# Optimization experiments

Measured on AMD Instinct MI355X. Metric: run time of the kernel, lower is better.

## Reference

```python
import jax, jax.numpy as jnp
import numpy as np

N_P, N_A = 100000, 20000
F_P, D_A, H = 512, 128, 256
E_W, E_C = 200000, 400000


def setup_inputs() -> dict:
    key = jax.random.key(0)
    ks = jax.random.split(key, 32)
    s = 0.05  # param init scale
    inp = {
        # node inputs
        'paper_feat': (jax.random.uniform(ks[0], (N_P, F_P)) < 0.02).astype(jnp.float32),  # sparse multi-hot
        'author_emb': jax.random.normal(ks[1], (N_A, D_A), jnp.float32),
        # edges: author --writes--> paper, paper --cites--> paper
        'writes_src': jax.random.randint(ks[2], (E_W,), 0, N_A, jnp.int32),
        'writes_dst': jax.random.randint(ks[3], (E_W,), 0, N_P, jnp.int32),
        'writes_w': jax.random.uniform(ks[4], (E_W,), jnp.float32),
        'cites_src': jax.random.randint(ks[5], (E_C,), 0, N_P, jnp.int32),
        'cites_dst': jax.random.randint(ks[6], (E_C,), 0, N_P, jnp.int32),
        'cites_w': jax.random.uniform(ks[7], (E_C,), jnp.float32),
        # layer 1 params (in dims per node type: paper=F_P, author=D_A)
        'W1_self_p': jax.random.normal(ks[8], (F_P, H), jnp.float32) * s,
        'b1_self_p': jnp.zeros((H,), jnp.float32),
        'W1_self_a': jax.random.normal(ks[9], (D_A, H), jnp.float32) * s,
        'b1_self_a': jnp.zeros((H,), jnp.float32),
        'W1_rel_writes': jax.random.normal(ks[10], (D_A, H), jnp.float32) * s,
        'b1_rel_writes': jnp.zeros((H,), jnp.float32),
        'W1_rel_cites': jax.random.normal(ks[11], (F_P, H), jnp.float32) * s,
        'b1_rel_cites': jnp.zeros((H,), jnp.float32),
        # layer 2 params (all in dims = H)
        'W2_self_p': jax.random.normal(ks[12], (H, H), jnp.float32) * s,
        'b2_self_p': jnp.zeros((H,), jnp.float32),
        'W2_self_a': jax.random.normal(ks[13], (H, H), jnp.float32) * s,
        'b2_self_a': jnp.zeros((H,), jnp.float32),
        'W2_rel_writes': jax.random.normal(ks[14], (H, H), jnp.float32) * s,
        'b2_rel_writes': jnp.zeros((H,), jnp.float32),
        'W2_rel_cites': jax.random.normal(ks[15], (H, H), jnp.float32) * s,
        'b2_rel_cites': jnp.zeros((H,), jnp.float32),
    }
    return inp


def _hetero_layer(xp, xa, edges, Wsp, bsp, Wsa, bsa, Wrw, brw, Wrc, brc, activation):
    """One HeteroLayer: per-type self linear + per-relation gather/scale/scatter-add."""
    writes_src, writes_dst, writes_w, cites_src, cites_dst, cites_w = edges
    out_p = xp @ Wsp + bsp          # [N_P, H]
    out_a = xa @ Wsa + bsa          # [N_A, H]
    # relation author --writes--> paper
    msg_w = xa @ Wrw + brw          # dense per-relation linear on source nodes
    gathered_w = msg_w[writes_src] * writes_w[:, None]          # gather + edge weight
    out_p = out_p + jax.ops.segment_sum(gathered_w, writes_dst, num_segments=out_p.shape[0])
    # relation paper --cites--> paper
    msg_c = xp @ Wrc + brc
    gathered_c = msg_c[cites_src] * cites_w[:, None]
    out_p = out_p + jax.ops.segment_sum(gathered_c, cites_dst, num_segments=out_p.shape[0])
    if activation:
        out_p = jax.nn.elu(out_p)
        out_a = jax.nn.elu(out_a)
    return out_p, out_a


def reference(paper_feat, author_emb,
              writes_src, writes_dst, writes_w,
              cites_src, cites_dst, cites_w,
              W1_self_p, b1_self_p, W1_self_a, b1_self_a,
              W1_rel_writes, b1_rel_writes, W1_rel_cites, b1_rel_cites,
              W2_self_p, b2_self_p, W2_self_a, b2_self_a,
              W2_rel_writes, b2_rel_writes, W2_rel_cites, b2_rel_cites):
    edges = (writes_src, writes_dst, writes_w, cites_src, cites_dst, cites_w)
    xp, xa = _hetero_layer(paper_feat, author_emb, edges,
                           W1_self_p, b1_self_p, W1_self_a, b1_self_a,
                           W1_rel_writes, b1_rel_writes, W1_rel_cites, b1_rel_cites,
                           activation=True)
    xp, xa = _hetero_layer(xp, xa, edges,
                           W2_self_p, b2_self_p, W2_self_a, b2_self_a,
                           W2_rel_writes, b2_rel_writes, W2_rel_cites, b2_rel_cites,
                           activation=False)
    return xp, xa
```

## Files before the change

kernel.cpp:

```cpp
#include <hip/hip_runtime.h>
#include <cstdint>
#include <cstddef>

constexpr int Hd  = 256;
constexpr int N_P = 100000;
constexpr int N_A = 20000;
constexpr int F_P = 512;
constexpr int D_A = 128;

typedef short bf16x8 __attribute__((ext_vector_type(8)));
typedef float f32x4  __attribute__((ext_vector_type(4)));

__device__ inline unsigned short f2b(float x) {
    unsigned u = __float_as_uint(x);
    u += 0x7fffu + ((u >> 16) & 1u);
    return (unsigned short)(u >> 16);
}
__device__ inline float b2f(unsigned short h) {
    return __uint_as_float((unsigned)h << 16);
}

__device__ inline void bsplit(float x, unsigned short& hi, unsigned short& lo) {
    const unsigned u = __float_as_uint(x);
    hi = (unsigned short)(u >> 16);
    const float r = x - __uint_as_float(u & 0xffff0000u);
    lo = (unsigned short)(__float_as_uint(r) >> 16);
}

__global__ void prep_kernel(const float* __restrict__ W1sa, const float* __restrict__ W1rw,
                            const float* __restrict__ W2sa, const float* __restrict__ W2rw,
                            const float* __restrict__ W2rc, const float* __restrict__ W2sp,
                            const float* __restrict__ b1sa, const float* __restrict__ b1rw,
                            const float* __restrict__ b2sa, const float* __restrict__ b2rw,
                            const float* __restrict__ b2rc, const float* __restrict__ b2sp,
                            unsigned short* __restrict__ w1h,  unsigned short* __restrict__ w1l,
                            unsigned short* __restrict__ wA2h, unsigned short* __restrict__ wA2l,
                            unsigned short* __restrict__ wP2h, unsigned short* __restrict__ wP2l,
                            float* __restrict__ bc1, float* __restrict__ bcA2,
                            float* __restrict__ bcP2) {
    const int b = blockIdx.x;
    if (b < 640) {
        const float *Wa, *Wb; unsigned short *wh, *wl; int rel;
        if (b < 128)      { Wa = W1sa; Wb = W1rw; wh = w1h;  wl = w1l;  rel = b; }
        else if (b < 384) { Wa = W2sa; Wb = W2rw; wh = wA2h; wl = wA2l; rel = b - 128; }
        else              { Wa = W2rc; Wb = W2sp; wh = wP2h; wl = wP2l; rel = b - 384; }
        const int ks  = rel >> 5;
        const int nfg = rel & 31;
        const int l   = threadIdx.x;
        const float* W = (nfg < 16) ? Wa : Wb;
        const int col  = (nfg & 15) * 16 + (l & 15);
        const size_t base = ((size_t)rel * 64 + l) * 8;
        #pragma unroll
        for (int j = 0; j < 8; ++j) {
            const int k = ks * 32 + ((l >> 4) * 8) + j;
            unsigned short h, lw;
            bsplit(W[(size_t)k * Hd + col], h, lw);
            wh[base + j] = h;
            wl[base + j] = lw;
        }
    } else {
        const int t     = (b - 640) * 64 + threadIdx.x;
        const int which = t >> 9;
        const int idx   = t & 511;
        const float* src; float* dst;
        if (which == 0)      { src = (idx < 256) ? b1sa : b1rw; dst = bc1; }
        else if (which == 1) { src = (idx < 256) ? b2sa : b2rw; dst = bcA2; }
        else                 { src = (idx < 256) ? b2rc : b2sp; dst = bcP2; }
        dst[idx] = src[idx & 255];
    }
}

__global__ void mfma_dual_kernel(const float* __restrict__ A, const int K,
                                 const unsigned short* __restrict__ whi,
                                 const unsigned short* __restrict__ wlo,
                                 const float* __restrict__ bcat,
                                 void* __restrict__ Oa, void* __restrict__ Ob,
                                 const int actA, const int actB,
                                 const int bfA, const int bfB) {
    extern __shared__ char smem[];
    char* sh = smem;
    char* sl = smem + 32 * K * 2;
    const int  tid = threadIdx.x;
    const int  wid = tid >> 6;
    const int  l   = tid & 63;
    const long m0  = (long)blockIdx.x * 32;
    const int  rowStride = 2 * K;

    const int kq4 = K >> 2;
    for (int i = tid; i < 32 * kq4; i += 256) {
        const int row = i / kq4;
        const int kq  = i - row * kq4;
        const float4 v = *(const float4*)(A + (m0 + row) * K + kq * 4);
        unsigned short h0, h1, h2, h3, l0, l1, l2, l3;
        bsplit(v.x, h0, l0); bsplit(v.y, h1, l1);
        bsplit(v.z, h2, l2); bsplit(v.w, h3, l3);
        int ofs = row * rowStride + ((kq * 8) ^ ((row & 7) << 4));
        *(ushort4*)(sh + ofs) = make_ushort4(h0, h1, h2, h3);
        *(ushort4*)(sl + ofs) = make_ushort4(l0, l1, l2, l3);
    }
    __syncthreads();

    f32x4 acc[2][8];
    #pragma unroll
    for (int nf = 0; nf < 8; ++nf) {
        const float b = bcat[wid * 128 + nf * 16 + (l & 15)];
        acc[0][nf] = (f32x4){b, b, b, b};
        acc[1][nf] = (f32x4){b, b, b, b};
    }

    const int kb  = (l >> 4) * 16;
    const int r0  = l & 15;
    const int r1  = 16 + r0;
    const int sw  = (l & 7) << 4;
    const int ro0 = r0 * rowStride;
    const int ro1 = r1 * rowStride;
    for (int ks = 0; ks < (K >> 5); ++ks) {
        const int bk = (ks * 64 + kb) ^ sw;
        const bf16x8 ah0 = *(const bf16x8*)(sh + ro0 + bk);
        const bf16x8 al0 = *(const bf16x8*)(sl + ro0 + bk);
        const bf16x8 ah1 = *(const bf16x8*)(sh + ro1 + bk);
        const bf16x8 al1 = *(const bf16x8*)(sl + ro1 + bk);
        const size_t wbase = (((size_t)ks * 32 + wid * 8) * 64 + l) * 8;
        #pragma unroll
        for (int nf = 0; nf < 8; ++nf) {
            const bf16x8 bh = *(const bf16x8*)(whi + wbase + (size_t)nf * 512);
            const bf16x8 bl = *(const bf16x8*)(wlo + wbase + (size_t)nf * 512);
            acc[0][nf] = __builtin_amdgcn_mfma_f32_16x16x32_bf16(ah0, bh, acc[0][nf], 0, 0, 0);
            acc[1][nf] = __builtin_amdgcn_mfma_f32_16x16x32_bf16(ah1, bh, acc[1][nf], 0, 0, 0);
            acc[0][nf] = __builtin_amdgcn_mfma_f32_16x16x32_bf16(al0, bh, acc[0][nf], 0, 0, 0);
            acc[1][nf] = __builtin_amdgcn_mfma_f32_16x16x32_bf16(al1, bh, acc[1][nf], 0, 0, 0);
            acc[0][nf] = __builtin_amdgcn_mfma_f32_16x16x32_bf16(ah0, bl, acc[0][nf], 0, 0, 0);
            acc[1][nf] = __builtin_amdgcn_mfma_f32_16x16x32_bf16(ah1, bl, acc[1][nf], 0, 0, 0);
        }
    }

    #pragma unroll
    for (int mf = 0; mf < 2; ++mf) {
        #pragma unroll
        for (int nf = 0; nf < 8; ++nf) {
            const int colg = wid * 128 + nf * 16 + (l & 15);
            void* O;
            int col, act, isbf;
            if (colg < 256) { O = Oa; col = colg;       act = actA; isbf = bfA; }
            else            { O = Ob; col = colg - 256; act = actB; isbf = bfB; }
            const long row = m0 + mf * 16 + ((l >> 4) * 4);
            const f32x4 v = acc[mf][nf];
            #pragma unroll
            for (int r = 0; r < 4; ++r) {
                float x = v[r];
                if (act) x = x > 0.f ? x : expm1f(x);
                if (isbf) ((unsigned short*)O)[(row + r) * Hd + col] = f2b(x);
                else      ((float*)O)[(row + r) * Hd + col] = x;
            }
        }
    }
}

__device__ inline void walk_row(const unsigned long long* __restrict__ m,
                                const float* __restrict__ Ws,
                                const float* __restrict__ Wc,
                                const int lane, float4& accS, float4& accC) {
    float4 pS = make_float4(0.f, 0.f, 0.f, 0.f);
    float4 pC = make_float4(0.f, 0.f, 0.f, 0.f);
    #pragma unroll
    for (int g = 0; g < 8; ++g) {
        const int cbase = (g >> 2) * 256 + (g & 3);
        unsigned long long mm = m[g];
        while (mm) {
            const int bit = __ffsll((long long)mm) - 1;
            mm &= mm - 1;
            const int k = cbase + bit * 4;
            const float4 nS = ((const float4*)(Ws + (size_t)k * Hd))[lane];
            const float4 nC = ((const float4*)(Wc + (size_t)k * Hd))[lane];
            accS.x += pS.x; accS.y += pS.y; accS.z += pS.z; accS.w += pS.w;
            accC.x += pC.x; accC.y += pC.y; accC.z += pC.z; accC.w += pC.w;
            pS = nS; pC = nC;
        }
    }
    accS.x += pS.x; accS.y += pS.y; accS.z += pS.z; accS.w += pS.w;
    accC.x += pC.x; accC.y += pC.y; accC.z += pC.z; accC.w += pC.w;
}

__global__ void sparse_dual_kernel(const float* __restrict__ pf,
                                   const float* __restrict__ Ws, const float* __restrict__ bs,
                                   const float* __restrict__ Wc, const float* __restrict__ bc,
                                   float* __restrict__ outS, unsigned short* __restrict__ outC) {
    const int lane = threadIdx.x & 63;
    const int row0 = blockIdx.x * 8 + (threadIdx.x >> 6) * 2;
    const float4* p0 = (const float4*)(pf + (size_t)row0 * F_P);
    const float4* p1 = (const float4*)(pf + (size_t)(row0 + 1) * F_P);
    const float4 a0 = p0[lane], b0 = p0[64 + lane];
    const float4 a1 = p1[lane], b1 = p1[64 + lane];
    unsigned long long m0[8], m1[8];
    m0[0] = __ballot(a0.x != 0.f); m0[1] = __ballot(a0.y != 0.f);
    m0[2] = __ballot(a0.z != 0.f); m0[3] = __ballot(a0.w != 0.f);
    m0[4] = __ballot(b0.x != 0.f); m0[5] = __ballot(b0.y != 0.f);
    m0[6] = __ballot(b0.z != 0.f); m0[7] = __ballot(b0.w != 0.f);
    m1[0] = __ballot(a1.x != 0.f); m1[1] = __ballot(a1.y != 0.f);
    m1[2] = __ballot(a1.z != 0.f); m1[3] = __ballot(a1.w != 0.f);
    m1[4] = __ballot(b1.x != 0.f); m1[5] = __ballot(b1.y != 0.f);
    m1[6] = __ballot(b1.z != 0.f); m1[7] = __ballot(b1.w != 0.f);

    const float4 biasS = ((const float4*)bs)[lane];
    const float4 biasC = ((const float4*)bc)[lane];

    float4 accS = biasS, accC = biasC;
    walk_row(m0, Ws, Wc, lane, accS, accC);
    ((float4*)(outS + (size_t)row0 * Hd))[lane] = accS;
    ((ushort4*)(outC + (size_t)row0 * Hd))[lane] =
        make_ushort4(f2b(accC.x), f2b(accC.y), f2b(accC.z), f2b(accC.w));

    accS = biasS; accC = biasC;
    walk_row(m1, Ws, Wc, lane, accS, accC);
    ((float4*)(outS + (size_t)(row0 + 1) * Hd))[lane] = accS;
    ((ushort4*)(outC + (size_t)(row0 + 1) * Hd))[lane] =
        make_ushort4(f2b(accC.x), f2b(accC.y), f2b(accC.z), f2b(accC.w));
}

__global__ void hist2_kernel(const int* __restrict__ wdst, const int EW,
                             const int* __restrict__ cdst, const int EC,
                             int* __restrict__ cntW, int* __restrict__ cntC) {
    for (int i = blockIdx.x * blockDim.x + threadIdx.x; i < EW + EC; i += gridDim.x * blockDim.x) {
        if (i < EW) atomicAdd(&cntW[wdst[i]], 1);
        else        atomicAdd(&cntC[cdst[i - EW]], 1);
    }
}

__global__ void scan1_kernel(int* __restrict__ offW, int* __restrict__ offC,
                             const int n, const int nb, int* __restrict__ bsum) {
    __shared__ int s[256];
    const int sec   = (blockIdx.x < nb) ? 0 : 1;
    int* data       = sec ? offC : offW;
    const int chunk = blockIdx.x - sec * nb;
    const int t = threadIdx.x;
    const int base = chunk * 1024 + t * 4;
    int v0 = (base + 0 < n) ? data[base + 0] : 0;
    int v1 = (base + 1 < n) ? data[base + 1] : 0;
    int v2 = (base + 2 < n) ? data[base + 2] : 0;
    int v3 = (base + 3 < n) ? data[base + 3] : 0;
    const int tsum = v0 + v1 + v2 + v3;
    s[t] = tsum;
    __syncthreads();
    for (int off = 1; off < 256; off <<= 1) {
        int y = (t >= off) ? s[t - off] : 0;
        __syncthreads();
        if (t >= off) s[t] += y;
        __syncthreads();
    }
    const int e = s[t] - tsum;
    if (base + 0 < n) data[base + 0] = e;
    if (base + 1 < n) data[base + 1] = e + v0;
    if (base + 2 < n) data[base + 2] = e + v0 + v1;
    if (base + 3 < n) data[base + 3] = e + v0 + v1 + v2;
    if (t == 255) bsum[blockIdx.x] = s[255];
}

__global__ void scan2_kernel(int* __restrict__ bsum, const int nb) {
    __shared__ int s[256];
    const int t = threadIdx.x;
    int* seg = bsum + blockIdx.x * nb;
    const int v = (t < nb) ? seg[t] : 0;
    s[t] = v;
    __syncthreads();
    for (int off = 1; off < 256; off <<= 1) {
        int y = (t >= off) ? s[t - off] : 0;
        __syncthreads();
        if (t >= off) s[t] += y;
        __syncthreads();
    }
    if (t < nb) seg[t] = s[t] - v;
}

__global__ void scan3_kernel(int* __restrict__ offW, int* __restrict__ offC,
                             const int n, const int nb, const int nblk,
                             const int* __restrict__ bsum) {
    const int sec = (blockIdx.x < nblk) ? 0 : 1;
    int* data     = sec ? offC : offW;
    const int i   = (blockIdx.x - sec * nblk) * 256 + threadIdx.x;
    if (i < n) data[i] += bsum[sec * nb + (i >> 10)];
}

__global__ void fill2_kernel(const int* __restrict__ wsrc, const int* __restrict__ wdst,
                             const float* __restrict__ ww, const int EW,
                             const int* __restrict__ csrc, const int* __restrict__ cdst,
                             const float* __restrict__ cw, const int EC,
                             int* __restrict__ curW, int* __restrict__ curC,
                             int2* __restrict__ edgeW, int2* __restrict__ edgeC) {
    for (int i = blockIdx.x * blockDim.x + threadIdx.x; i < EW + EC; i += gridDim.x * blockDim.x) {
        if (i < EW) {
            const int p = atomicAdd(&curW[wdst[i]], 1);
            edgeW[p] = make_int2(wsrc[i], __float_as_int(ww[i]));
        } else {
            const int j = i - EW;
            const int p = atomicAdd(&curC[cdst[j]], 1);
            edgeC[p] = make_int2(csrc[j], __float_as_int(cw[j]));
        }
    }
}

__device__ inline void fma4(float4& acc, const float w, const ushort4 q) {
    acc.x += w * b2f(q.x); acc.y += w * b2f(q.y);
    acc.z += w * b2f(q.z); acc.w += w * b2f(q.w);
}

__device__ inline void gather_rel(float4& acc, const int lane,
                                  const unsigned short* __restrict__ m,
                                  const int2* __restrict__ earr,
                                  const int s, const int e) {
    int i = s;
    int2 e0, e1;
    if (i + 2 <= e) { e0 = earr[i]; e1 = earr[i + 1]; }
    ushort4 q0 = make_ushort4(0, 0, 0, 0), q1 = q0;
    float w0 = 0.f, w1 = 0.f;
    int havePend = 0;
    while (i + 2 <= e) {
        const ushort4 g0 = ((const ushort4*)(m + (size_t)e0.x * Hd))[lane];
        const ushort4 g1 = ((const ushort4*)(m + (size_t)e1.x * Hd))[lane];
        const float cw0 = __int_as_float(e0.y);
        const float cw1 = __int_as_float(e1.y);
        i += 2;
        if (i + 2 <= e) { e0 = earr[i]; e1 = earr[i + 1]; }
        if (havePend) { fma4(acc, w0, q0); fma4(acc, w1, q1); }
        q0 = g0; q1 = g1; w0 = cw0; w1 = cw1; havePend = 1;
    }
    if (havePend) { fma4(acc, w0, q0); fma4(acc, w1, q1); }
    for (; i < e; ++i) {
        const int2 ee = earr[i];
        const ushort4 g = ((const ushort4*)(m + (size_t)ee.x * Hd))[lane];
        fma4(acc, __int_as_float(ee.y), g);
    }
}

__global__ void aggregate_kernel(float* __restrict__ io,
                                 const unsigned short* __restrict__ mW, const int* __restrict__ offW,
                                 const int2* __restrict__ eW,
                                 const unsigned short* __restrict__ mC, const int* __restrict__ offC,
                                 const int2* __restrict__ eC,
                                 const int do_elu) {
    const int wid  = threadIdx.x >> 6;
    const int lane = threadIdx.x & 63;
    const int p    = blockIdx.x * 4 + wid;
    if (p >= N_P) return;
    float4 acc = ((const float4*)(io + (size_t)p * Hd))[lane];
    gather_rel(acc, lane, mW, eW, (p == 0) ? 0 : offW[p - 1], offW[p]);
    gather_rel(acc, lane, mC, eC, (p == 0) ? 0 : offC[p - 1], offC[p]);
    if (do_elu) {
        acc.x = acc.x > 0.f ? acc.x : expm1f(acc.x);
        acc.y = acc.y > 0.f ? acc.y : expm1f(acc.y);
        acc.z = acc.z > 0.f ? acc.z : expm1f(acc.z);
        acc.w = acc.w > 0.f ? acc.w : expm1f(acc.w);
    }
    ((float4*)(io + (size_t)p * Hd))[lane] = acc;
}

extern "C" void kernel_launch(void* const* d_in, const int* in_sizes, int n_in,
                              void* d_out, int out_size, void* d_ws, size_t ws_size,
                              hipStream_t stream) {
    const float* pf    = (const float*)d_in[0];
    const float* ae    = (const float*)d_in[1];
    const int*   wsrc  = (const int*)d_in[2];
    const int*   wdst  = (const int*)d_in[3];
    const float* ww    = (const float*)d_in[4];
    const int*   csrc  = (const int*)d_in[5];
    const int*   cdst  = (const int*)d_in[6];
    const float* cw    = (const float*)d_in[7];
    const float* W1sp  = (const float*)d_in[8];
    const float* b1sp  = (const float*)d_in[9];
    const float* W1sa  = (const float*)d_in[10];
    const float* b1sa  = (const float*)d_in[11];
    const float* W1rw  = (const float*)d_in[12];
    const float* b1rw  = (const float*)d_in[13];
    const float* W1rc  = (const float*)d_in[14];
    const float* b1rc  = (const float*)d_in[15];
    const float* W2sp  = (const float*)d_in[16];
    const float* b2sp  = (const float*)d_in[17];
    const float* W2sa  = (const float*)d_in[18];
    const float* b2sa  = (const float*)d_in[19];
    const float* W2rw  = (const float*)d_in[20];
    const float* b2rw  = (const float*)d_in[21];
    const float* W2rc  = (const float*)d_in[22];
    const float* b2rc  = (const float*)d_in[23];

    const int E_W = in_sizes[2];
    const int E_C = in_sizes[5];

    float* outP = (float*)d_out;
    float* outA = outP + (size_t)N_P * Hd;

    float*          xa1    = (float*)d_ws;
    unsigned short* msgw_b = (unsigned short*)(xa1 + (size_t)N_A * Hd);
    unsigned short* msg_b  = msgw_b + (size_t)N_A * Hd;
    int*            offW   = (int*)(msg_b + (size_t)N_P * Hd);
    int*            offC   = offW + N_P;
    int2*           edgeW  = (int2*)(offC + N_P);
    int2*           edgeC  = edgeW + E_W;
    int*            bsum   = (int*)(edgeC + E_C);
    float*          bc1    = (float*)(bsum + 512);
    float*          bcA2   = bc1 + 512;
    float*          bcP2   = bcA2 + 512;
    unsigned short* w1h    = (unsigned short*)(bcP2 + 512);
    unsigned short* w1l    = w1h  + (size_t)128 * 512;
    unsigned short* wA2h   = w1l  + (size_t)128 * 512;
    unsigned short* wA2l   = wA2h + (size_t)256 * 512;
    unsigned short* wP2h   = wA2l + (size_t)256 * 512;
    unsigned short* wP2l   = wP2h + (size_t)256 * 512;

    const dim3 blk(256);
    const int  nb   = (N_P + 1023) / 1024;
    const int  nblk = (N_P + 255) / 256;

    prep_kernel<<<664, 64, 0, stream>>>(W1sa, W1rw, W2sa, W2rw, W2rc, W2sp,
                                        b1sa, b1rw, b2sa, b2rw, b2rc, b2sp,
                                        w1h, w1l, wA2h, wA2l, wP2h, wP2l,
                                        bc1, bcA2, bcP2);

    hipMemsetAsync(offW, 0, (size_t)2 * N_P * sizeof(int), stream);
    hist2_kernel<<<1024, blk, 0, stream>>>(wdst, E_W, cdst, E_C, offW, offC);
    scan1_kernel<<<2 * nb, blk, 0, stream>>>(offW, offC, N_P, nb, bsum);
    scan2_kernel<<<2, blk, 0, stream>>>(bsum, nb);
    scan3_kernel<<<2 * nblk, blk, 0, stream>>>(offW, offC, N_P, nb, nblk, bsum);
    fill2_kernel<<<1024, blk, 0, stream>>>(wsrc, wdst, ww, E_W, csrc, cdst, cw, E_C,
                                           offW, offC, edgeW, edgeC);

    sparse_dual_kernel<<<N_P / 8, blk, 0, stream>>>(pf, W1sp, b1sp, W1rc, b1rc, outP, msg_b);
    mfma_dual_kernel<<<N_A / 32, blk, 128 * 128, stream>>>(ae, 128, w1h, w1l, bc1,
                                                           xa1, msgw_b, 1, 0, 0, 1);
    aggregate_kernel<<<(N_P + 3) / 4, blk, 0, stream>>>(outP, msgw_b, offW, edgeW,
                                                        msg_b, offC, edgeC, 1);

    mfma_dual_kernel<<<N_A / 32, blk, 128 * 256, stream>>>(xa1, 256, wA2h, wA2l, bcA2,
                                                           outA, msgw_b, 0, 0, 0, 1);
    mfma_dual_kernel<<<N_P / 32, blk, 128 * 256, stream>>>(outP, 256, wP2h, wP2l, bcP2,
                                                           msg_b, outP, 0, 0, 1, 0);
    aggregate_kernel<<<(N_P + 3) / 4, blk, 0, stream>>>(outP, msgw_b, offW, edgeW,
                                                        msg_b, offC, edgeC, 0);
}
```

Baseline: 544.5 us.

## Merge edge CSR, compact sparse nonzeros, stage edges in LDS, bf16 cites weight

The two relations' CSR structures are merged into one edge list over a concatenated author+paper message buffer. This halves the histogram, scan and fill work and gives aggregation one contiguous edge range per node. The aggregate kernel stages each block's edges in shared memory and gathers four messages per chunk with double buffering to raise memory-level parallelism. The sparse first layer packs each wave's nonzero indices for four rows into an LDS queue and walks them in pipelined chunks. It also reads a bf16 copy of W1_rel_cites, adding bf16 rounding of that weight and extra prep work.

```diff
diff --git a/kernel.cpp b/kernel.cpp
--- a/kernel.cpp
+++ b/kernel.cpp
@@ -11,16 +11,16 @@
 typedef short bf16x8 __attribute__((ext_vector_type(8)));
 typedef float f32x4  __attribute__((ext_vector_type(4)));
 
-__device__ inline unsigned short f2b(float x) {
+__device__ __forceinline__ unsigned short f2b(float x) {
     unsigned u = __float_as_uint(x);
     u += 0x7fffu + ((u >> 16) & 1u);
     return (unsigned short)(u >> 16);
 }
-__device__ inline float b2f(unsigned short h) {
+__device__ __forceinline__ float b2f(unsigned short h) {
     return __uint_as_float((unsigned)h << 16);
 }
 
-__device__ inline void bsplit(float x, unsigned short& hi, unsigned short& lo) {
+__device__ __forceinline__ void bsplit(float x, unsigned short& hi, unsigned short& lo) {
     const unsigned u = __float_as_uint(x);
     hi = (unsigned short)(u >> 16);
     const float r = x - __uint_as_float(u & 0xffff0000u);
@@ -30,12 +30,14 @@
 __global__ void prep_kernel(const float* __restrict__ W1sa, const float* __restrict__ W1rw,
                             const float* __restrict__ W2sa, const float* __restrict__ W2rw,
                             const float* __restrict__ W2rc, const float* __restrict__ W2sp,
+                            const float* __restrict__ W1rc,
                             const float* __restrict__ b1sa, const float* __restrict__ b1rw,
                             const float* __restrict__ b2sa, const float* __restrict__ b2rw,
                             const float* __restrict__ b2rc, const float* __restrict__ b2sp,
                             unsigned short* __restrict__ w1h,  unsigned short* __restrict__ w1l,
                             unsigned short* __restrict__ wA2h, unsigned short* __restrict__ wA2l,
                             unsigned short* __restrict__ wP2h, unsigned short* __restrict__ wP2l,
+                            unsigned short* __restrict__ wcb,
                             float* __restrict__ bc1, float* __restrict__ bcA2,
                             float* __restrict__ bcP2) {
     const int b = blockIdx.x;
@@ -58,8 +60,12 @@
             wh[base + j] = h;
             wl[base + j] = lw;
         }
+    } else if (b < 896) {
+        const int i0 = (b - 640) * 512 + threadIdx.x * 8;
+        #pragma unroll
+        for (int j = 0; j < 8; ++j) wcb[i0 + j] = f2b(W1rc[i0 + j]);
     } else {
-        const int t     = (b - 640) * 64 + threadIdx.x;
+        const int t     = (b - 896) * 64 + threadIdx.x;
         const int which = t >> 9;
         const int idx   = t & 511;
         const float* src; float* dst;
@@ -156,84 +162,139 @@
     }
 }
 
-__device__ inline void walk_row(const unsigned long long* __restrict__ m,
-                                const float* __restrict__ Ws,
-                                const float* __restrict__ Wc,
-                                const int lane, float4& accS, float4& accC) {
-    float4 pS = make_float4(0.f, 0.f, 0.f, 0.f);
-    float4 pC = make_float4(0.f, 0.f, 0.f, 0.f);
-    #pragma unroll
-    for (int g = 0; g < 8; ++g) {
-        const int cbase = (g >> 2) * 256 + (g & 3);
-        unsigned long long mm = m[g];
-        while (mm) {
-            const int bit = __ffsll((long long)mm) - 1;
-            mm &= mm - 1;
-            const int k = cbase + bit * 4;
-            const float4 nS = ((const float4*)(Ws + (size_t)k * Hd))[lane];
-            const float4 nC = ((const float4*)(Wc + (size_t)k * Hd))[lane];
-            accS.x += pS.x; accS.y += pS.y; accS.z += pS.z; accS.w += pS.w;
-            accC.x += pC.x; accC.y += pC.y; accC.z += pC.z; accC.w += pC.w;
-            pS = nS; pC = nC;
-        }
-    }
-    accS.x += pS.x; accS.y += pS.y; accS.z += pS.z; accS.w += pS.w;
-    accC.x += pC.x; accC.y += pC.y; accC.z += pC.z; accC.w += pC.w;
+struct SpChunk {
+    float4  s0, s1, s2, s3;
+    ushort4 c0, c1, c2, c3;
+    float   f0, f1, f2, f3;
+    int     r0, r1, r2, r3;
+};
+
+__device__ __forceinline__ void sp_issue(const unsigned short* __restrict__ wq, const int chunk,
+                                         const float* __restrict__ Ws,
+                                         const unsigned short* __restrict__ Wc,
+                                         const int lane, SpChunk& C) {
+    const ushort4 ee = *(const ushort4*)(wq + chunk * 4);
+#define SP_ONE(EV, SS, CC, FF, RR) { \
+    const int ent = (int)(EV); const int k = ent & 511; \
+    FF = (ent & 2048) ? 0.f : 1.f; \
+    RR = (ent >> 9) & 3; \
+    SS = ((const float4*)(Ws + (size_t)k * Hd))[lane]; \
+    CC = ((const ushort4*)(Wc + (size_t)k * Hd))[lane]; }
+    SP_ONE(ee.x, C.s0, C.c0, C.f0, C.r0)
+    SP_ONE(ee.y, C.s1, C.c1, C.f1, C.r1)
+    SP_ONE(ee.z, C.s2, C.c2, C.f2, C.r2)
+    SP_ONE(ee.w, C.s3, C.c3, C.f3, C.r3)
+#undef SP_ONE
+}
+
+__device__ __forceinline__ void acc1(float4& aS, float4& aC,
+                                     const float4 ws, const ushort4 wc, const float f) {
+    aS.x = fmaf(f, ws.x, aS.x); aS.y = fmaf(f, ws.y, aS.y);
+    aS.z = fmaf(f, ws.z, aS.z); aS.w = fmaf(f, ws.w, aS.w);
+    aC.x = fmaf(f, b2f(wc.x), aC.x); aC.y = fmaf(f, b2f(wc.y), aC.y);
+    aC.z = fmaf(f, b2f(wc.z), aC.z); aC.w = fmaf(f, b2f(wc.w), aC.w);
+}
+
+__device__ __forceinline__ void sp_acc(const SpChunk& C,
+        float4& aS0, float4& aC0, float4& aS1, float4& aC1,
+        float4& aS2, float4& aC2, float4& aS3, float4& aC3) {
+#define SP_A(RR, SS, CC, FF) \
+    if (RR == 0)      acc1(aS0, aC0, SS, CC, FF); \
+    else if (RR == 1) acc1(aS1, aC1, SS, CC, FF); \
+    else if (RR == 2) acc1(aS2, aC2, SS, CC, FF); \
+    else              acc1(aS3, aC3, SS, CC, FF);
+    SP_A(C.r0, C.s0, C.c0, C.f0)
+    SP_A(C.r1, C.s1, C.c1, C.f1)
+    SP_A(C.r2, C.s2, C.c2, C.f2)
+    SP_A(C.r3, C.s3, C.c3, C.f3)
+#undef SP_A
 }
 
 __global__ void sparse_dual_kernel(const float* __restrict__ pf,
                                    const float* __restrict__ Ws, const float* __restrict__ bs,
-                                   const float* __restrict__ Wc, const float* __restrict__ bc,
+                                   const unsigned short* __restrict__ Wc, const float* __restrict__ bc,
                                    float* __restrict__ outS, unsigned short* __restrict__ outC) {
+    __shared__ unsigned short q[4][2048];
     const int lane = threadIdx.x & 63;
-    const int row0 = blockIdx.x * 8 + (threadIdx.x >> 6) * 2;
-    const float4* p0 = (const float4*)(pf + (size_t)row0 * F_P);
-    const float4* p1 = (const float4*)(pf + (size_t)(row0 + 1) * F_P);
-    const float4 a0 = p0[lane], b0 = p0[64 + lane];
-    const float4 a1 = p1[lane], b1 = p1[64 + lane];
-    unsigned long long m0[8], m1[8];
-    m0[0] = __ballot(a0.x != 0.f); m0[1] = __ballot(a0.y != 0.f);
-    m0[2] = __ballot(a0.z != 0.f); m0[3] = __ballot(a0.w != 0.f);
-    m0[4] = __ballot(b0.x != 0.f); m0[5] = __ballot(b0.y != 0.f);
-    m0[6] = __ballot(b0.z != 0.f); m0[7] = __ballot(b0.w != 0.f);
-    m1[0] = __ballot(a1.x != 0.f); m1[1] = __ballot(a1.y != 0.f);
-    m1[2] = __ballot(a1.z != 0.f); m1[3] = __ballot(a1.w != 0.f);
-    m1[4] = __ballot(b1.x != 0.f); m1[5] = __ballot(b1.y != 0.f);
-    m1[6] = __ballot(b1.z != 0.f); m1[7] = __ballot(b1.w != 0.f);
-
-    const float4 biasS = ((const float4*)bs)[lane];
-    const float4 biasC = ((const float4*)bc)[lane];
-
-    float4 accS = biasS, accC = biasC;
-    walk_row(m0, Ws, Wc, lane, accS, accC);
-    ((float4*)(outS + (size_t)row0 * Hd))[lane] = accS;
-    ((ushort4*)(outC + (size_t)row0 * Hd))[lane] =
-        make_ushort4(f2b(accC.x), f2b(accC.y), f2b(accC.z), f2b(accC.w));
-
-    accS = biasS; accC = biasC;
-    walk_row(m1, Ws, Wc, lane, accS, accC);
-    ((float4*)(outS + (size_t)(row0 + 1) * Hd))[lane] = accS;
-    ((ushort4*)(outC + (size_t)(row0 + 1) * Hd))[lane] =
-        make_ushort4(f2b(accC.x), f2b(accC.y), f2b(accC.z), f2b(accC.w));
-}
-
-__global__ void hist2_kernel(const int* __restrict__ wdst, const int EW,
-                             const int* __restrict__ cdst, const int EC,
-                             int* __restrict__ cntW, int* __restrict__ cntC) {
+    const int wid  = threadIdx.x >> 6;
+    const long r0  = (long)blockIdx.x * 16 + wid * 4;
+    unsigned short* wq = q[wid];
+
+    const float4* p0 = (const float4*)(pf + (r0 + 0) * F_P);
+    const float4* p1 = (const float4*)(pf + (r0 + 1) * F_P);
+    const float4* p2 = (const float4*)(pf + (r0 + 2) * F_P);
+    const float4* p3 = (const float4*)(pf + (r0 + 3) * F_P);
+    const float4 A0 = p0[lane], B0 = p0[64 + lane];
+    const float4 A1 = p1[lane], B1 = p1[64 + lane];
+    const float4 A2 = p2[lane], B2 = p2[64 + lane];
+    const float4 A3 = p3[lane], B3 = p3[64 + lane];
+
+    int qn = 0;
+#define SP_GRP(VAL, KOFS, ROW) { \
+    const bool nz = (VAL) != 0.f; \
+    const unsigned long long mk = __ballot(nz); \
+    if (nz) { \
+        const int within = __builtin_amdgcn_mbcnt_hi((unsigned)(mk >> 32), \
+                           __builtin_amdgcn_mbcnt_lo((unsigned)mk, 0)); \
+        wq[qn + within] = (unsigned short)(((KOFS) + lane * 4) | ((ROW) << 9)); \
+    } \
+    qn += (int)__popcll(mk); }
+    SP_GRP(A0.x, 0,   0) SP_GRP(A0.y, 1,   0) SP_GRP(A0.z, 2,   0) SP_GRP(A0.w, 3,   0)
+    SP_GRP(B0.x, 256, 0) SP_GRP(B0.y, 257, 0) SP_GRP(B0.z, 258, 0) SP_GRP(B0.w, 259, 0)
+    SP_GRP(A1.x, 0,   1) SP_GRP(A1.y, 1,   1) SP_GRP(A1.z, 2,   1) SP_GRP(A1.w, 3,   1)
+    SP_GRP(B1.x, 256, 1) SP_GRP(B1.y, 257, 1) SP_GRP(B1.z, 258, 1) SP_GRP(B1.w, 259, 1)
+    SP_GRP(A2.x, 0,   2) SP_GRP(A2.y, 1,   2) SP_GRP(A2.z, 2,   2) SP_GRP(A2.w, 3,   2)
+    SP_GRP(B2.x, 256, 2) SP_GRP(B2.y, 257, 2) SP_GRP(B2.z, 258, 2) SP_GRP(B2.w, 259, 2)
+    SP_GRP(A3.x, 0,   3) SP_GRP(A3.y, 1,   3) SP_GRP(A3.z, 2,   3) SP_GRP(A3.w, 3,   3)
+    SP_GRP(B3.x, 256, 3) SP_GRP(B3.y, 257, 3) SP_GRP(B3.z, 258, 3) SP_GRP(B3.w, 259, 3)
+#undef SP_GRP
+    const int qnp = (qn + 7) & ~7;
+    if (lane < qnp - qn) wq[qn + lane] = 0x0800;
+
+    float4 aS0 = ((const float4*)bs)[lane];
+    float4 aC0 = ((const float4*)bc)[lane];
+    float4 aS1 = aS0, aS2 = aS0, aS3 = aS0;
+    float4 aC1 = aC0, aC2 = aC0, aC3 = aC0;
+
+    if (qn > 0) {
+        const int nc = qnp >> 2;
+        SpChunk CA, CB;
+        sp_issue(wq, 0, Ws, Wc, lane, CA);
+        int c = 1;
+        for (; c + 1 < nc; c += 2) {
+            sp_issue(wq, c, Ws, Wc, lane, CB);
+            sp_acc(CA, aS0, aC0, aS1, aC1, aS2, aC2, aS3, aC3);
+            sp_issue(wq, c + 1, Ws, Wc, lane, CA);
+            sp_acc(CB, aS0, aC0, aS1, aC1, aS2, aC2, aS3, aC3);
+        }
+        sp_issue(wq, nc - 1, Ws, Wc, lane, CB);
+        sp_acc(CA, aS0, aC0, aS1, aC1, aS2, aC2, aS3, aC3);
+        sp_acc(CB, aS0, aC0, aS1, aC1, aS2, aC2, aS3, aC3);
+    }
+
+    ((float4*)(outS + (r0 + 0) * Hd))[lane] = aS0;
+    ((float4*)(outS + (r0 + 1) * Hd))[lane] = aS1;
+    ((float4*)(outS + (r0 + 2) * Hd))[lane] = aS2;
+    ((float4*)(outS + (r0 + 3) * Hd))[lane] = aS3;
+    ((ushort4*)(outC + (r0 + 0) * Hd))[lane] = make_ushort4(f2b(aC0.x), f2b(aC0.y), f2b(aC0.z), f2b(aC0.w));
+    ((ushort4*)(outC + (r0 + 1) * Hd))[lane] = make_ushort4(f2b(aC1.x), f2b(aC1.y), f2b(aC1.z), f2b(aC1.w));
+    ((ushort4*)(outC + (r0 + 2) * Hd))[lane] = make_ushort4(f2b(aC2.x), f2b(aC2.y), f2b(aC2.z), f2b(aC2.w));
+    ((ushort4*)(outC + (r0 + 3) * Hd))[lane] = make_ushort4(f2b(aC3.x), f2b(aC3.y), f2b(aC3.z), f2b(aC3.w));
+}
+
+__global__ void hist_kernel(const int* __restrict__ wdst, const int EW,
+                            const int* __restrict__ cdst, const int EC,
+                            int* __restrict__ cnt) {
     for (int i = blockIdx.x * blockDim.x + threadIdx.x; i < EW + EC; i += gridDim.x * blockDim.x) {
-        if (i < EW) atomicAdd(&cntW[wdst[i]], 1);
-        else        atomicAdd(&cntC[cdst[i - EW]], 1);
-    }
-}
-
-__global__ void scan1_kernel(int* __restrict__ offW, int* __restrict__ offC,
-                             const int n, const int nb, int* __restrict__ bsum) {
+        const int d = (i < EW) ? wdst[i] : cdst[i - EW];
+        atomicAdd(&cnt[d], 1);
+    }
+}
+
+__global__ void scan1_kernel(int* __restrict__ data, const int n, int* __restrict__ bsum) {
     __shared__ int s[256];
-    const int sec   = (blockIdx.x < nb) ? 0 : 1;
-    int* data       = sec ? offC : offW;
-    const int chunk = blockIdx.x - sec * nb;
     const int t = threadIdx.x;
-    const int base = chunk * 1024 + t * 4;
+    const int base = blockIdx.x * 1024 + t * 4;
     int v0 = (base + 0 < n) ? data[base + 0] : 0;
     int v1 = (base + 1 < n) ? data[base + 1] : 0;
     int v2 = (base + 2 < n) ? data[base + 2] : 0;
@@ -258,8 +319,7 @@
 __global__ void scan2_kernel(int* __restrict__ bsum, const int nb) {
     __shared__ int s[256];
     const int t = threadIdx.x;
-    int* seg = bsum + blockIdx.x * nb;
-    const int v = (t < nb) ? seg[t] : 0;
+    const int v = (t < nb) ? bsum[t] : 0;
     s[t] = v;
     __syncthreads();
     for (int off = 1; off < 256; off <<= 1) {
@@ -268,82 +328,102 @@
         if (t >= off) s[t] += y;
         __syncthreads();
     }
-    if (t < nb) seg[t] = s[t] - v;
-}
-
-__global__ void scan3_kernel(int* __restrict__ offW, int* __restrict__ offC,
-                             const int n, const int nb, const int nblk,
-                             const int* __restrict__ bsum) {
-    const int sec = (blockIdx.x < nblk) ? 0 : 1;
-    int* data     = sec ? offC : offW;
-    const int i   = (blockIdx.x - sec * nblk) * 256 + threadIdx.x;
-    if (i < n) data[i] += bsum[sec * nb + (i >> 10)];
-}
-
-__global__ void fill2_kernel(const int* __restrict__ wsrc, const int* __restrict__ wdst,
-                             const float* __restrict__ ww, const int EW,
-                             const int* __restrict__ csrc, const int* __restrict__ cdst,
-                             const float* __restrict__ cw, const int EC,
-                             int* __restrict__ curW, int* __restrict__ curC,
-                             int2* __restrict__ edgeW, int2* __restrict__ edgeC) {
+    if (t < nb) bsum[t] = s[t] - v;
+}
+
+__global__ void scan3_kernel(int* __restrict__ data, const int n, const int* __restrict__ bsum) {
+    const int i = blockIdx.x * blockDim.x + threadIdx.x;
+    if (i < n) data[i] += bsum[i >> 10];
+}
+
+__global__ void fill_kernel(const int* __restrict__ wsrc, const int* __restrict__ wdst,
+                            const float* __restrict__ ww, const int EW,
+                            const int* __restrict__ csrc, const int* __restrict__ cdst,
+                            const float* __restrict__ cw, const int EC,
+                            int* __restrict__ cur, int2* __restrict__ edges) {
     for (int i = blockIdx.x * blockDim.x + threadIdx.x; i < EW + EC; i += gridDim.x * blockDim.x) {
-        if (i < EW) {
-            const int p = atomicAdd(&curW[wdst[i]], 1);
-            edgeW[p] = make_int2(wsrc[i], __float_as_int(ww[i]));
-        } else {
-            const int j = i - EW;
-            const int p = atomicAdd(&curC[cdst[j]], 1);
-            edgeC[p] = make_int2(csrc[j], __float_as_int(cw[j]));
-        }
-    }
-}
-
-__device__ inline void fma4(float4& acc, const float w, const ushort4 q) {
-    acc.x += w * b2f(q.x); acc.y += w * b2f(q.y);
-    acc.z += w * b2f(q.z); acc.w += w * b2f(q.w);
-}
-
-__device__ inline void gather_rel(float4& acc, const int lane,
-                                  const unsigned short* __restrict__ m,
-                                  const int2* __restrict__ earr,
-                                  const int s, const int e) {
-    int i = s;
-    int2 e0, e1;
-    if (i + 2 <= e) { e0 = earr[i]; e1 = earr[i + 1]; }
-    ushort4 q0 = make_ushort4(0, 0, 0, 0), q1 = q0;
-    float w0 = 0.f, w1 = 0.f;
-    int havePend = 0;
-    while (i + 2 <= e) {
-        const ushort4 g0 = ((const ushort4*)(m + (size_t)e0.x * Hd))[lane];
-        const ushort4 g1 = ((const ushort4*)(m + (size_t)e1.x * Hd))[lane];
-        const float cw0 = __int_as_float(e0.y);
-        const float cw1 = __int_as_float(e1.y);
-        i += 2;
-        if (i + 2 <= e) { e0 = earr[i]; e1 = earr[i + 1]; }
-        if (havePend) { fma4(acc, w0, q0); fma4(acc, w1, q1); }
-        q0 = g0; q1 = g1; w0 = cw0; w1 = cw1; havePend = 1;
-    }
-    if (havePend) { fma4(acc, w0, q0); fma4(acc, w1, q1); }
-    for (; i < e; ++i) {
-        const int2 ee = earr[i];
-        const ushort4 g = ((const ushort4*)(m + (size_t)ee.x * Hd))[lane];
-        fma4(acc, __int_as_float(ee.y), g);
-    }
+        int d, sp; float w;
+        if (i < EW) { d = wdst[i]; sp = wsrc[i]; w = ww[i]; }
+        else        { const int j = i - EW; d = cdst[j]; sp = N_A + csrc[j]; w = cw[j]; }
+        const int p = atomicAdd(&cur[d], 1);
+        edges[p] = make_int2(sp, __float_as_int(w));
+    }
+}
+
+struct AgChunk { ushort4 g0, g1, g2, g3; float w0, w1, w2, w3; };
+
+__device__ __forceinline__ void ag_issue(const int2* __restrict__ eq, const int base, const int n,
+                                         const unsigned short* __restrict__ msg,
+                                         const int lane, AgChunk& C) {
+#define AG_ONE(J, GG, WW) { \
+    const int idx = base + (J); \
+    const int2 ee = eq[min(idx, n - 1)]; \
+    WW = (idx < n) ? __int_as_float(ee.y) : 0.f; \
+    GG = ((const ushort4*)(msg + (size_t)ee.x * Hd))[lane]; }
+    AG_ONE(0, C.g0, C.w0)
+    AG_ONE(1, C.g1, C.w1)
+    AG_ONE(2, C.g2, C.w2)
+    AG_ONE(3, C.g3, C.w3)
+#undef AG_ONE
+}
+
+__device__ __forceinline__ void ag_acc(const AgChunk& C, float4& acc) {
+#define AG_A(GG, WW) { \
+    acc.x = fmaf(WW, b2f(GG.x), acc.x); acc.y = fmaf(WW, b2f(GG.y), acc.y); \
+    acc.z = fmaf(WW, b2f(GG.z), acc.z); acc.w = fmaf(WW, b2f(GG.w), acc.w); }
+    AG_A(C.g0, C.w0) AG_A(C.g1, C.w1) AG_A(C.g2, C.w2) AG_A(C.g3, C.w3)
+#undef AG_A
 }
 
 __global__ void aggregate_kernel(float* __restrict__ io,
-                                 const unsigned short* __restrict__ mW, const int* __restrict__ offW,
-                                 const int2* __restrict__ eW,
-                                 const unsigned short* __restrict__ mC, const int* __restrict__ offC,
-                                 const int2* __restrict__ eC,
+                                 const unsigned short* __restrict__ msgAll,
+                                 const int* __restrict__ off,
+                                 const int2* __restrict__ edges,
                                  const int do_elu) {
+    __shared__ int2 eq[1024];
     const int wid  = threadIdx.x >> 6;
     const int lane = threadIdx.x & 63;
-    const int p    = blockIdx.x * 4 + wid;
-    if (p >= N_P) return;
+    const int p0   = blockIdx.x * 4;
+    const int sAll = (p0 == 0) ? 0 : off[p0 - 1];
+    const int tot  = off[p0 + 3] - sAll;
+    const bool fits = (tot <= 1024);
+    if (fits)
+        for (int i = threadIdx.x; i < tot; i += 256) eq[i] = edges[sAll + i];
+    __syncthreads();
+
+    const int p = p0 + wid;
+    const int s = (p == 0) ? 0 : off[p - 1];
+    const int e = off[p];
+    const int n = e - s;
     float4 acc = ((const float4*)(io + (size_t)p * Hd))[lane];
-    gather_rel(acc, lane, mW, eW, (p == 0) ? 0 : offW[p - 1], offW[p]);
-    gather_rel(acc, lane, mC, eC, (p == 0) ? 0 : offC[p - 1], offC[p]);
+
+    if (n > 0) {
+        if (fits) {
+            const int2* eqw = eq + (s - sAll);
+            int nc = (n + 3) >> 2;
+            nc += (nc & 1);
+            AgChunk CA, CB;
+            ag_issue(eqw, 0, n, msgAll, lane, CA);
+            int c = 1;
+            for (; c + 1 < nc; c += 2) {
+                ag_issue(eqw, 4 * c, n, msgAll, lane, CB);
+                ag_acc(CA, acc);
+                ag_issue(eqw, 4 * (c + 1), n, msgAll, lane, CA);
+                ag_acc(CB, acc);
+            }
+            ag_issue(eqw, 4 * (nc - 1), n, msgAll, lane, CB);
+            ag_acc(CA, acc);
+            ag_acc(CB, acc);
+        } else {
+            for (int i = s; i < e; ++i) {
+                const int2 ee = edges[i];
+                const ushort4 g = ((const ushort4*)(msgAll + (size_t)ee.x * Hd))[lane];
+                const float w = __int_as_float(ee.y);
+                acc.x = fmaf(w, b2f(g.x), acc.x); acc.y = fmaf(w, b2f(g.y), acc.y);
+                acc.z = fmaf(w, b2f(g.z), acc.z); acc.w = fmaf(w, b2f(g.w), acc.w);
+            }
+        }
+    }
     if (do_elu) {
         acc.x = acc.x > 0.f ? acc.x : expm1f(acc.x);
         acc.y = acc.y > 0.f ? acc.y : expm1f(acc.y);
@@ -388,14 +468,12 @@
     float* outA = outP + (size_t)N_P * Hd;
 
     float*          xa1    = (float*)d_ws;
-    unsigned short* msgw_b = (unsigned short*)(xa1 + (size_t)N_A * Hd);
-    unsigned short* msg_b  = msgw_b + (size_t)N_A * Hd;
-    int*            offW   = (int*)(msg_b + (size_t)N_P * Hd);
-    int*            offC   = offW + N_P;
-    int2*           edgeW  = (int2*)(offC + N_P);
-    int2*           edgeC  = edgeW + E_W;
-    int*            bsum   = (int*)(edgeC + E_C);
-    float*          bc1    = (float*)(bsum + 512);
+    unsigned short* msgAll = (unsigned short*)(xa1 + (size_t)N_A * Hd);
+    unsigned short* msgP   = msgAll + (size_t)N_A * Hd;
+    int*            off    = (int*)(msgAll + (size_t)(N_A + N_P) * Hd);
+    int2*           edges  = (int2*)(off + N_P);
+    int*            bsum   = (int*)(edges + (E_W + E_C));
+    float*          bc1    = (float*)(bsum + 256);
     float*          bcA2   = bc1 + 512;
     float*          bcP2   = bcA2 + 512;
     unsigned short* w1h    = (unsigned short*)(bcP2 + 512);
@@ -404,34 +482,33 @@
     unsigned short* wA2l   = wA2h + (size_t)256 * 512;
     unsigned short* wP2h   = wA2l + (size_t)256 * 512;
     unsigned short* wP2l   = wP2h + (size_t)256 * 512;
+    unsigned short* wcb    = wP2l + (size_t)256 * 512;
 
     const dim3 blk(256);
-    const int  nb   = (N_P + 1023) / 1024;
-    const int  nblk = (N_P + 255) / 256;
-
-    prep_kernel<<<664, 64, 0, stream>>>(W1sa, W1rw, W2sa, W2rw, W2rc, W2sp,
+    const int  nb = (N_P + 1023) / 1024;
+
+    prep_kernel<<<920, 64, 0, stream>>>(W1sa, W1rw, W2sa, W2rw, W2rc, W2sp, W1rc,
                                         b1sa, b1rw, b2sa, b2rw, b2rc, b2sp,
-                                        w1h, w1l, wA2h, wA2l, wP2h, wP2l,
+                                        w1h, w1l, wA2h, wA2l, wP2h, wP2l, wcb,
                                         bc1, bcA2, bcP2);
 
-    hipMemsetAsync(offW, 0, (size_t)2 * N_P * sizeof(int), stream);
-    hist2_kernel<<<1024, blk, 0, stream>>>(wdst, E_W, cdst, E_C, offW, offC);
-    scan1_kernel<<<2 * nb, blk, 0, stream>>>(offW, offC, N_P, nb, bsum);
-    scan2_kernel<<<2, blk, 0, stream>>>(bsum, nb);
-    scan3_kernel<<<2 * nblk, blk, 0, stream>>>(offW, offC, N_P, nb, nblk, bsum);
-    fill2_kernel<<<1024, blk, 0, stream>>>(wsrc, wdst, ww, E_W, csrc, cdst, cw, E_C,
-                                           offW, offC, edgeW, edgeC);
-
-    sparse_dual_kernel<<<N_P / 8, blk, 0, stream>>>(pf, W1sp, b1sp, W1rc, b1rc, outP, msg_b);
+    hipMemsetAsync(off, 0, (size_t)N_P * sizeof(int), stream);
+    hist_kernel<<<1024, blk, 0, stream>>>(wdst, E_W, cdst, E_C, off);
+    scan1_kernel<<<nb, blk, 0, stream>>>(off, N_P, bsum);
+    scan2_kernel<<<1,  blk, 0, stream>>>(bsum, nb);
+    scan3_kernel<<<(N_P + 255) / 256, blk, 0, stream>>>(off, N_P, bsum);
+    fill_kernel<<<1024, blk, 0, stream>>>(wsrc, wdst, ww, E_W, csrc, cdst, cw, E_C,
+                                          off, edges);
+
+    sparse_dual_kernel<<<N_P / 16, blk, 0, stream>>>(pf, W1sp, b1sp, wcb, b1rc,
+                                                     outP, msgP);
     mfma_dual_kernel<<<N_A / 32, blk, 128 * 128, stream>>>(ae, 128, w1h, w1l, bc1,
-                                                           xa1, msgw_b, 1, 0, 0, 1);
-    aggregate_kernel<<<(N_P + 3) / 4, blk, 0, stream>>>(outP, msgw_b, offW, edgeW,
-                                                        msg_b, offC, edgeC, 1);
+                                                           xa1, msgAll, 1, 0, 0, 1);
+    aggregate_kernel<<<N_P / 4, blk, 0, stream>>>(outP, msgAll, off, edges, 1);
 
     mfma_dual_kernel<<<N_A / 32, blk, 128 * 256, stream>>>(xa1, 256, wA2h, wA2l, bcA2,
-                                                           outA, msgw_b, 0, 0, 0, 1);
+                                                           outA, msgAll, 0, 0, 0, 1);
     mfma_dual_kernel<<<N_P / 32, blk, 128 * 256, stream>>>(outP, 256, wP2h, wP2l, bcP2,
-                                                           msg_b, outP, 0, 0, 1, 0);
-    aggregate_kernel<<<(N_P + 3) / 4, blk, 0, stream>>>(outP, msgw_b, offW, edgeW,
-                                                        msg_b, offC, edgeC, 0);
-}
+                                                           msgP, outP, 0, 0, 1, 0);
+    aggregate_kernel<<<N_P / 4, blk, 0, stream>>>(outP, msgAll, off, edges, 0);
+}
```

Result: slower. 778.0 us (+42.9%).
